# Optimization experiments

Measured on AMD Instinct MI355X. Metric: run time of the kernel, lower is better.

## Reference

```python
import jax, jax.numpy as jnp
import numpy as np

NEG_INF = -1e9  # matches torch masked_fill(-1000000000.0)


def setup_inputs() -> dict:
    key = jax.random.key(0)
    kv, kk, kq, km, kw, kb = jax.random.split(key, 6)
    B, Lq, Lk, D = 8, 1024, 4096, 1024  # Lq must equal D (transpose-then-merge quirk)
    v = jax.random.normal(kv, (B, Lk, D), dtype=jnp.float32)
    k = jax.random.normal(kk, (B, Lk, D), dtype=jnp.float32)
    q = jax.random.normal(kq, (B, Lq, D), dtype=jnp.float32)
    mask = jax.random.randint(km, (B, Lq, Lk), 0, 2) > 0  # bool, True = masked out
    W_merge = jax.random.normal(kw, (D, D), dtype=jnp.float32) / np.sqrt(D)
    b_merge = jax.random.normal(kb, (D,), dtype=jnp.float32) * 0.02
    return {"v": v, "k": k, "q": q, "mask": mask, "W_merge": W_merge, "b_merge": b_merge}


def reference(v, k, q, mask, W_merge, b_merge):
    d_k = q.shape[-1]
    scale = 1.0 / jnp.sqrt(jnp.asarray(d_k, dtype=q.dtype))
    # scores: [B, Lq, Lk]
    scores = jnp.einsum('bqd,bkd->bqk', q, k) * scale
    scores = jnp.where(mask, jnp.asarray(NEG_INF, dtype=scores.dtype), scores)
    att_map = jax.nn.softmax(scores, axis=-1)  # dropout = identity in eval
    atted = jnp.einsum('bqk,bkd->bqd', att_map, v)  # [B, Lq, D]
    atted = jnp.swapaxes(atted, -1, -2)  # [B, D, Lq]; Lq == hid_dim
    # nn.Linear: y = x @ W^T + b
    return jnp.einsum('bdl,ol->bdo', atted, W_merge) + b_merge
```

## Files before the change

### kernel.cpp

```cpp
#include <hip/hip_runtime.h>
#include <stdint.h>

typedef __attribute__((ext_vector_type(4))) float f32x4;
typedef __attribute__((ext_vector_type(8))) short bf16x8;
typedef __attribute__((ext_vector_type(4))) short bf16x4v;
typedef __attribute__((ext_vector_type(4))) unsigned int u32x4;

#define NBATCH 8
#define LQS    1024
#define LKS    4096
#define DDIM   1024
#define QKSCALE 0.03125f
#define NEGINF -1000000000.0f
#define BK 64

__device__ __forceinline__ short f2bf(float x) {
    unsigned u = __builtin_bit_cast(unsigned, x);
    unsigned r = (u + 0x7fffu + ((u >> 16) & 1u)) >> 16;
    return (short)r;
}

__device__ __forceinline__ bf16x8 cvt8(const float* f) {
    const u32x4* u = (const u32x4*)f;
    const u32x4 a = u[0], b = u[1];
    union { unsigned w[4]; bf16x8 v; } c;
    c.w[0] = __builtin_amdgcn_perm(a[1], a[0], 0x07060302u);
    c.w[1] = __builtin_amdgcn_perm(a[3], a[2], 0x07060302u);
    c.w[2] = __builtin_amdgcn_perm(b[1], b[0], 0x07060302u);
    c.w[3] = __builtin_amdgcn_perm(b[3], b[2], 0x07060302u);
    return c.v;
}

__device__ __forceinline__ void g2l16(const void* g, void* lds) {
    __builtin_amdgcn_global_load_lds(
        (const __attribute__((address_space(1))) unsigned int*)g,
        (__attribute__((address_space(3))) unsigned int*)lds,
        16, 0, 0);
}

__global__ void detect_kernel(const unsigned char* __restrict__ mb,
                              int* __restrict__ flags) {
    if (threadIdx.x != 0 || blockIdx.x != 0) return;
    int is_i32 = 1;
    for (int i = 0; i < 256; ++i) {
        if ((i & 3) != 0 && mb[i] != 0) { is_i32 = 0; break; }
    }
    flags[0] = is_i32;
}

__global__ __launch_bounds__(256) void cvt_kernel(
    const float* __restrict__ src, short* __restrict__ dst, int n8) {
    const int stride = gridDim.x * 256;
    for (int i = blockIdx.x * 256 + threadIdx.x; i < n8; i += stride)
        ((bf16x8*)dst)[i] = cvt8(src + (size_t)i * 8);
}

__global__ __launch_bounds__(256) void transv_kernel(
    const float* __restrict__ V, short* __restrict__ VT) {
    __shared__ short LDSt[64 * 72];
    const int tid = threadIdx.x;
    const int cb  = blockIdx.x >> 10;
    const int t   = blockIdx.x & 1023;
    const int kt  = t >> 4, dt = t & 15;
    const int k0  = kt * 64, d0 = dt * 64;
    const float* Vb  = V  + (size_t)cb * LKS * DDIM;
    short*       VTb = VT + (size_t)cb * ((size_t)DDIM * LKS);

    const int r  = tid >> 4;
    const int cp = (tid & 15) * 4;
#pragma unroll
    for (int rr = 0; rr < 4; ++rr) {
        const int row = rr * 16 + r;
        const f32x4 v = *(const f32x4*)(Vb + (size_t)(k0 + row) * DDIM + d0 + cp);
#pragma unroll
        for (int i = 0; i < 4; ++i) LDSt[(cp + i) * 72 + row] = f2bf(v[i]);
    }
    __syncthreads();
    const int dr = tid >> 2;
    const int kq = (tid & 3) * 16;
    const bf16x8 o0 = *(const bf16x8*)&LDSt[dr * 72 + kq];
    const bf16x8 o1 = *(const bf16x8*)&LDSt[dr * 72 + kq + 8];
    short* dst = VTb + (size_t)(d0 + dr) * LKS + k0 + kq;
    *(bf16x8*)dst       = o0;
    *(bf16x8*)(dst + 8) = o1;
}


__device__ __forceinline__ void stage_half(const short* gbase, int ld,
                                           short* ldshalf, int tid) {
    const int r0 = tid >> 3;
    const int gc = (tid & 7) ^ (r0 & 7);
    const short* s0 = gbase + (size_t)r0 * ld + gc * 8;
    const short* s1 = gbase + (size_t)(r0 + 64) * ld + gc * 8;
    g2l16(s0, ldshalf + (tid & 0x1C0) * 8);
    g2l16(s1, ldshalf + 4096 + (tid & 0x1C0) * 8);
}

__device__ __forceinline__ bf16x8 rdfrag(const short* lds, int base, int r, int c) {
    return *(const bf16x8*)&lds[base + r * 64 + ((c ^ (r & 7)) << 3)];
}

#define MFMA16(d, a, b) d = __builtin_amdgcn_mfma_f32_16x16x32_bf16(a, b, d, 0, 0, 0)

#define PHASE(MF0, STAGE, TAIL)                                             \
    {                                                                       \
        bf16x8 a00 = rdfrag(lds, aBase, (MF0) * 16 + lo, g);                \
        bf16x8 a01 = rdfrag(lds, aBase, (MF0) * 16 + lo, 4 + g);            \
        bf16x8 a10 = rdfrag(lds, aBase, (MF0) * 16 + 16 + lo, g);           \
        bf16x8 a11 = rdfrag(lds, aBase, (MF0) * 16 + 16 + lo, 4 + g);       \
        STAGE;                                                              \
        asm volatile("s_barrier" ::: "memory");                             \
        __builtin_amdgcn_s_setprio(1);                                      \
        _Pragma("unroll")                                                   \
        for (int nf = 0; nf < 4; ++nf) {                                    \
            MFMA16(acc[(MF0)][nf], a00, bfr[nf][0]);                        \
            MFMA16(acc[(MF0)][nf], a01, bfr[nf][1]);                        \
            MFMA16(acc[(MF0) + 1][nf], a10, bfr[nf][0]);                    \
            MFMA16(acc[(MF0) + 1][nf], a11, bfr[nf][1]);                    \
        }                                                                   \
        __builtin_amdgcn_s_setprio(0);                                      \
        TAIL;                                                               \
        asm volatile("s_barrier" ::: "memory");                             \
    }

template <int EPI>
__device__ __forceinline__ void gemm8p_body(
    const short* __restrict__ A, int lda,
    const short* __restrict__ B, int ldb,
    void* __restrict__ C, int ldc,
    const float* __restrict__ bias,
    int m0, int n0, int NK, float scale, short* lds) {

    const int tid = threadIdx.x;
    const int w = tid >> 6, lane = tid & 63;
    const int lo = lane & 15, g = lane >> 4;
    const int wr = w >> 2, wc = w & 3;

    const short* gA0 = A + (size_t)m0 * lda;
    const short* gA1 = A + (size_t)(m0 + 128) * lda;
    const short* gB0 = B + (size_t)n0 * ldb;
    const short* gB1 = B + (size_t)(n0 + 128) * ldb;

    f32x4 acc[8][4];
#pragma unroll
    for (int mf = 0; mf < 8; ++mf)
#pragma unroll
        for (int nf = 0; nf < 4; ++nf) acc[mf][nf] = (f32x4){0.f, 0.f, 0.f, 0.f};

    stage_half(gA0, lda, lds + 0,     tid);
    stage_half(gA1, lda, lds + 8192,  tid);
    stage_half(gB0, ldb, lds + 16384, tid);
    stage_half(gB1, ldb, lds + 24576, tid);
    stage_half(gB0 + BK, ldb, lds + 32768 + 16384, tid);
    stage_half(gB1 + BK, ldb, lds + 32768 + 24576, tid);
    asm volatile("s_waitcnt vmcnt(4)" ::: "memory");
    asm volatile("s_barrier" ::: "memory");

    for (int kt = 0; kt < NK; ++kt) {
        const int cb = (kt & 1) << 15;
        const int ob = cb ^ 32768;
        const int aBase = cb + wr * 8192;
        const int bBase = cb + 16384 + (wc >> 1) * 8192;
        const int brow  = (wc & 1) * 64;
        const int kA = (kt + 1) * BK, kB = (kt + 2) * BK;
        const bool doA = (kt + 1) < NK, doB = (kt + 2) < NK;

        bf16x8 bfr[4][2];
#pragma unroll
        for (int nf = 0; nf < 4; ++nf) {
            bfr[nf][0] = rdfrag(lds, bBase, brow + nf * 16 + lo, g);
            bfr[nf][1] = rdfrag(lds, bBase, brow + nf * 16 + lo, 4 + g);
        }
        PHASE(0, if (doA) stage_half(gA0 + kA, lda, lds + ob, tid), )
        PHASE(2, if (doA) stage_half(gA1 + kA, lda, lds + ob + 8192, tid), )
        PHASE(4, if (doB) stage_half(gB0 + kB, ldb, lds + cb + 16384, tid), )
        PHASE(6, if (doB) stage_half(gB1 + kB, ldb, lds + cb + 24576, tid),
                 asm volatile("s_waitcnt vmcnt(4)" ::: "memory"))
    }

#pragma unroll
    for (int nf = 0; nf < 4; ++nf) {
        const int col = n0 + wc * 64 + nf * 16 + lo;
        float bv = 0.f;
        if constexpr (EPI == 2) bv = bias[col];
#pragma unroll
        for (int mf = 0; mf < 8; ++mf) {
#pragma unroll
            for (int rr = 0; rr < 4; ++rr) {
                const size_t oa =
                    (size_t)(m0 + wr * 128 + mf * 16 + g * 4 + rr) * ldc + col;
                if constexpr (EPI == 0)      ((float*)C)[oa] = acc[mf][nf][rr] * scale;
                else if constexpr (EPI == 1) ((short*)C)[oa] = f2bf(acc[mf][nf][rr]);
                else                         ((float*)C)[oa] = acc[mf][nf][rr] + bv;
            }
        }
    }
}

__global__ __launch_bounds__(512, 2) void gemm1_kernel(
    const short* __restrict__ Qb, const short* __restrict__ Kb,
    float* __restrict__ S) {
    __shared__ __align__(16) short lds[65536];
    const int cb = blockIdx.x >> 6;
    const int t  = blockIdx.x & 63;
    gemm8p_body<0>(Qb + (size_t)cb * LQS * DDIM, DDIM,
                   Kb + (size_t)cb * LKS * DDIM, DDIM,
                   S + (size_t)cb * ((size_t)LQS * LKS), LKS, nullptr,
                   (t >> 4) * 256, (t & 15) * 256, DDIM / BK, QKSCALE, lds);
}

__global__ __launch_bounds__(512, 2) void gemm2_kernel(
    const short* __restrict__ VT, const short* __restrict__ Pd,
    short* __restrict__ attedT) {
    __shared__ __align__(16) short lds[65536];
    const int cb = blockIdx.x >> 4;
    const int t  = blockIdx.x & 15;
    gemm8p_body<1>(VT + (size_t)cb * ((size_t)DDIM * LKS), LKS,
                   Pd + (size_t)cb * ((size_t)LQS * LKS), LKS,
                   attedT + (size_t)cb * ((size_t)DDIM * LQS), LQS, nullptr,
                   (t >> 2) * 256, (t & 3) * 256, LKS / BK, 1.f, lds);
}

__global__ __launch_bounds__(512, 2) void merge_kernel(
    const short* __restrict__ attedT, const short* __restrict__ Wb,
    const float* __restrict__ bias, float* __restrict__ out) {
    __shared__ __align__(16) short lds[65536];
    const int mt = blockIdx.x >> 2;
    const int nt = blockIdx.x & 3;
    gemm8p_body<2>(attedT, DDIM, Wb, DDIM, out, DDIM, bias,
                   mt * 256, nt * 256, DDIM / BK, 1.f, lds);
}

__global__ __launch_bounds__(256) void softmax_kernel(
    const float* __restrict__ S, short* __restrict__ Pd,
    const void* __restrict__ mask, const int* __restrict__ flags, int c0) {
    __shared__ float red[4];
    const int tid = threadIdx.x, w = tid >> 6, lane = tid & 63;
    const int cb = blockIdx.x >> 10;
    const int q  = blockIdx.x & 1023;
    const int mflag = flags[0];

    const float* Srow = S + ((size_t)cb * LQS + q) * LKS;
    const size_t roff = ((size_t)(c0 + cb) * LQS + q) * LKS;

    float sc[16];
#pragma unroll
    for (int j = 0; j < 4; ++j) {
        const f32x4 sv = ((const f32x4*)Srow)[j * 256 + tid];
        int m0, m1, m2, m3;
        if (mflag) {
            const int4 mv = ((const int4*)((const int*)mask + roff))[j * 256 + tid];
            m0 = mv.x; m1 = mv.y; m2 = mv.z; m3 = mv.w;
        } else {
            const uchar4 mv = ((const uchar4*)((const unsigned char*)mask + roff))[j * 256 + tid];
            m0 = mv.x; m1 = mv.y; m2 = mv.z; m3 = mv.w;
        }
        sc[j * 4 + 0] = m0 ? NEGINF : sv[0];
        sc[j * 4 + 1] = m1 ? NEGINF : sv[1];
        sc[j * 4 + 2] = m2 ? NEGINF : sv[2];
        sc[j * 4 + 3] = m3 ? NEGINF : sv[3];
    }

    float lm = -INFINITY;
#pragma unroll
    for (int i = 0; i < 16; ++i) lm = fmaxf(lm, sc[i]);
#pragma unroll
    for (int off = 1; off < 64; off <<= 1) lm = fmaxf(lm, __shfl_xor(lm, off));
    if (lane == 0) red[w] = lm;
    __syncthreads();
    const float m = fmaxf(fmaxf(red[0], red[1]), fmaxf(red[2], red[3]));

    float p[16], ls = 0.f;
#pragma unroll
    for (int i = 0; i < 16; ++i) { p[i] = __expf(sc[i] - m); ls += p[i]; }
#pragma unroll
    for (int off = 1; off < 64; off <<= 1) ls += __shfl_xor(ls, off);
    __syncthreads();
    if (lane == 0) red[w] = ls;
    __syncthreads();
    const float inv = 1.f / (red[0] + red[1] + red[2] + red[3]);

    short* Prow = Pd + ((size_t)cb * LQS + q) * LKS;
#pragma unroll
    for (int j = 0; j < 4; ++j) {
        bf16x4v pv;
#pragma unroll
        for (int i = 0; i < 4; ++i) pv[i] = f2bf(p[j * 4 + i] * inv);
        ((bf16x4v*)Prow)[j * 256 + tid] = pv;
    }
}

extern "C" void kernel_launch(void* const* d_in, const int* in_sizes, int n_in,
                              void* d_out, int out_size, void* d_ws, size_t ws_size,
                              hipStream_t stream) {
    const float* v    = (const float*)d_in[0];
    const float* k    = (const float*)d_in[1];
    const float* q    = (const float*)d_in[2];
    const void*  mask = d_in[3];
    const float* Wm   = (const float*)d_in[4];
    const float* bias = (const float*)d_in[5];
    float* out = (float*)d_out;

    const size_t base = 4096 + (2ull << 20);
    int nb = 0;
    for (int cand = 8; cand >= 1; cand >>= 1)
        if (base + (size_t)cand * (36ull << 20) <= ws_size) { nb = cand; break; }
    if (!nb) return;

    int*   flags = (int*)d_ws;
    short* Wb    = (short*)((char*)d_ws + 4096);
    char*  ar    = (char*)d_ws + base;
    float* Sbuf   = (float*)ar;
    short* VTbuf  = (short*)(ar + ((size_t)nb << 24));
    short* attedT = (short*)(ar + ((size_t)nb << 24) + ((size_t)nb << 23));
    short* Qb     = (short*)(ar + ((size_t)nb << 24) + ((size_t)nb << 23) + ((size_t)nb << 21));
    short* Kb     = (short*)(ar + ((size_t)nb << 24) + ((size_t)nb << 23) + 2 * ((size_t)nb << 21));
    short* Pd     = Kb;

    hipLaunchKernelGGL(detect_kernel, dim3(1), dim3(64), 0, stream,
                       (const unsigned char*)mask, flags);
    hipLaunchKernelGGL(cvt_kernel, dim3(512), dim3(256), 0, stream,
                       Wm, Wb, (int)(DDIM * DDIM / 8));

    for (int c0 = 0; c0 < NBATCH; c0 += nb) {
        const float* vc = v + (size_t)c0 * LKS * DDIM;
        const float* kc = k + (size_t)c0 * LKS * DDIM;
        const float* qc = q + (size_t)c0 * LQS * DDIM;
        float*       oc = out + (size_t)c0 * DDIM * LQS;

        hipLaunchKernelGGL(cvt_kernel, dim3(1024), dim3(256), 0, stream,
                           qc, Qb, nb * (LQS * DDIM / 8));
        hipLaunchKernelGGL(cvt_kernel, dim3(2048), dim3(256), 0, stream,
                           kc, Kb, nb * (LKS * DDIM / 8));
        hipLaunchKernelGGL(transv_kernel, dim3(nb * 1024), dim3(256), 0, stream,
                           vc, VTbuf);
        hipLaunchKernelGGL(gemm1_kernel, dim3(nb * 64), dim3(512), 0, stream,
                           Qb, Kb, Sbuf);
        hipLaunchKernelGGL(softmax_kernel, dim3(nb * 1024), dim3(256), 0, stream,
                           Sbuf, Pd, mask, flags, c0);
        hipLaunchKernelGGL(gemm2_kernel, dim3(nb * 16), dim3(512), 0, stream,
                           VTbuf, Pd, attedT);
        hipLaunchKernelGGL(merge_kernel, dim3(nb * 4 * 4), dim3(512), 0, stream,
                           attedT, Wb, bias, oc);
    }
}
```

Measured before the change: 382.3 us.

## Split-K the PV GEMM across two blocks and swizzle blocks across XCDs

The P·V GEMM now splits its K=4096 reduction into two halves. That doubles the grid from nb*16 to nb*32 workgroups so the GPU's CUs are better filled. Each half writes fp32 partials into the reused score buffer, and a new add2 kernel sums them and converts to bf16 for the merge GEMM. All three GEMM kernels also remap block IDs with an XCD swizzle so neighbouring tiles land on the same chiplet for L2 reuse, and the pipeline tail now waits with vmcnt(0) when no B prefetch was issued. The cost is an extra kernel launch plus fp32 partial traffic.

New measurement: 367.1 us. 4.0% less time.

```diff
diff --git a/kernel.cpp b/kernel.cpp
--- a/kernel.cpp
+++ b/kernel.cpp
@@ -38,6 +38,10 @@
         16, 0, 0);
 }
 
+__device__ __forceinline__ int xcd_swz(int bid, int nwg) {
+    return (bid & 7) * (nwg >> 3) + (bid >> 3);
+}
+
 __global__ void detect_kernel(const unsigned char* __restrict__ mb,
                               int* __restrict__ flags) {
     if (threadIdx.x != 0 || blockIdx.x != 0) return;
@@ -53,6 +57,24 @@
     const int stride = gridDim.x * 256;
     for (int i = blockIdx.x * 256 + threadIdx.x; i < n8; i += stride)
         ((bf16x8*)dst)[i] = cvt8(src + (size_t)i * 8);
+}
+
+__global__ __launch_bounds__(256) void add2_kernel(
+    const float* __restrict__ p0, const float* __restrict__ p1,
+    short* __restrict__ dst, int n8) {
+    const int stride = gridDim.x * 256;
+    for (int i = blockIdx.x * 256 + threadIdx.x; i < n8; i += stride) {
+        const f32x4 a0 = ((const f32x4*)p0)[2 * i];
+        const f32x4 a1 = ((const f32x4*)p0)[2 * i + 1];
+        const f32x4 b0 = ((const f32x4*)p1)[2 * i];
+        const f32x4 b1 = ((const f32x4*)p1)[2 * i + 1];
+        bf16x8 r;
+#pragma unroll
+        for (int j = 0; j < 4; ++j) r[j]     = f2bf(a0[j] + b0[j]);
+#pragma unroll
+        for (int j = 0; j < 4; ++j) r[4 + j] = f2bf(a1[j] + b1[j]);
+        ((bf16x8*)dst)[i] = r;
+    }
 }
 
 __global__ __launch_bounds__(256) void transv_kernel(
@@ -85,7 +107,6 @@
     *(bf16x8*)(dst + 8) = o1;
 }
 
-
 __device__ __forceinline__ void stage_half(const short* gbase, int ld,
                                            short* ldshalf, int tid) {
     const int r0 = tid >> 3;
@@ -106,8 +127,8 @@
     {                                                                       \
         bf16x8 a00 = rdfrag(lds, aBase, (MF0) * 16 + lo, g);                \
         bf16x8 a01 = rdfrag(lds, aBase, (MF0) * 16 + lo, 4 + g);            \
-        bf16x8 a10 = rdfrag(lds, aBase, (MF0) * 16 + 16 + lo, g);           \
-        bf16x8 a11 = rdfrag(lds, aBase, (MF0) * 16 + 16 + lo, 4 + g);       \
+        bf16x8 a10 = rdfrag(lds, aBase, (MF0) * 16 + 16 + lo, g);          \
+        bf16x8 a11 = rdfrag(lds, aBase, (MF0) * 16 + 16 + lo, 4 + g);      \
         STAGE;                                                              \
         asm volatile("s_barrier" ::: "memory");                             \
         __builtin_amdgcn_s_setprio(1);                                      \
@@ -175,7 +196,10 @@
         PHASE(2, if (doA) stage_half(gA1 + kA, lda, lds + ob + 8192, tid), )
         PHASE(4, if (doB) stage_half(gB0 + kB, ldb, lds + cb + 16384, tid), )
         PHASE(6, if (doB) stage_half(gB1 + kB, ldb, lds + cb + 24576, tid),
-                 asm volatile("s_waitcnt vmcnt(4)" ::: "memory"))
+                 {
+                     if (doB) { asm volatile("s_waitcnt vmcnt(4)" ::: "memory"); }
+                     else     { asm volatile("s_waitcnt vmcnt(0)" ::: "memory"); }
+                 })
     }
 
 #pragma unroll
@@ -201,8 +225,9 @@
     const short* __restrict__ Qb, const short* __restrict__ Kb,
     float* __restrict__ S) {
     __shared__ __align__(16) short lds[65536];
-    const int cb = blockIdx.x >> 6;
-    const int t  = blockIdx.x & 63;
+    const int bid = xcd_swz(blockIdx.x, gridDim.x);
+    const int cb = bid >> 6;
+    const int t  = bid & 63;
     gemm8p_body<0>(Qb + (size_t)cb * LQS * DDIM, DDIM,
                    Kb + (size_t)cb * LKS * DDIM, DDIM,
                    S + (size_t)cb * ((size_t)LQS * LKS), LKS, nullptr,
@@ -211,22 +236,26 @@
 
 __global__ __launch_bounds__(512, 2) void gemm2_kernel(
     const short* __restrict__ VT, const short* __restrict__ Pd,
-    short* __restrict__ attedT) {
+    float* __restrict__ Cpart, int nb) {
     __shared__ __align__(16) short lds[65536];
-    const int cb = blockIdx.x >> 4;
-    const int t  = blockIdx.x & 15;
-    gemm8p_body<1>(VT + (size_t)cb * ((size_t)DDIM * LKS), LKS,
-                   Pd + (size_t)cb * ((size_t)LQS * LKS), LKS,
-                   attedT + (size_t)cb * ((size_t)DDIM * LQS), LQS, nullptr,
-                   (t >> 2) * 256, (t & 3) * 256, LKS / BK, 1.f, lds);
+    const int bid = xcd_swz(blockIdx.x, gridDim.x);
+    const int cb = bid >> 5;
+    const int t  = (bid >> 1) & 15;
+    const int s  = bid & 1;
+    float* Cp = Cpart + (size_t)s * nb * (1 << 20) + (size_t)cb * (1 << 20);
+    gemm8p_body<0>(VT + (size_t)cb * ((size_t)DDIM * LKS) + s * 2048, LKS,
+                   Pd + (size_t)cb * ((size_t)LQS * LKS) + s * 2048, LKS,
+                   Cp, LQS, nullptr,
+                   (t >> 2) * 256, (t & 3) * 256, 2048 / BK, 1.f, lds);
 }
 
 __global__ __launch_bounds__(512, 2) void merge_kernel(
     const short* __restrict__ attedT, const short* __restrict__ Wb,
     const float* __restrict__ bias, float* __restrict__ out) {
     __shared__ __align__(16) short lds[65536];
-    const int mt = blockIdx.x >> 2;
-    const int nt = blockIdx.x & 3;
+    const int bid = xcd_swz(blockIdx.x, gridDim.x);
+    const int mt = bid >> 2;
+    const int nt = bid & 3;
     gemm8p_body<2>(attedT, DDIM, Wb, DDIM, out, DDIM, bias,
                    mt * 256, nt * 256, DDIM / BK, 1.f, lds);
 }
@@ -316,6 +345,7 @@
     short* Qb     = (short*)(ar + ((size_t)nb << 24) + ((size_t)nb << 23) + ((size_t)nb << 21));
     short* Kb     = (short*)(ar + ((size_t)nb << 24) + ((size_t)nb << 23) + 2 * ((size_t)nb << 21));
     short* Pd     = Kb;
+    float* Cpart  = Sbuf;
 
     hipLaunchKernelGGL(detect_kernel, dim3(1), dim3(64), 0, stream,
                        (const unsigned char*)mask, flags);
@@ -338,9 +368,12 @@
                            Qb, Kb, Sbuf);
         hipLaunchKernelGGL(softmax_kernel, dim3(nb * 1024), dim3(256), 0, stream,
                            Sbuf, Pd, mask, flags, c0);
-        hipLaunchKernelGGL(gemm2_kernel, dim3(nb * 16), dim3(512), 0, stream,
-                           VTbuf, Pd, attedT);
-        hipLaunchKernelGGL(merge_kernel, dim3(nb * 4 * 4), dim3(512), 0, stream,
+        hipLaunchKernelGGL(gemm2_kernel, dim3(nb * 32), dim3(512), 0, stream,
+                           VTbuf, Pd, Cpart, nb);
+        hipLaunchKernelGGL(add2_kernel, dim3(1024), dim3(256), 0, stream,
+                           Cpart, Cpart + (size_t)nb * (1 << 20), attedT,
+                           nb * (1 << 17));
+        hipLaunchKernelGGL(merge_kernel, dim3(nb * 16), dim3(512), 0, stream,
                            attedT, Wb, bias, oc);
     }
 }
```
